# Performance work log

Measured on AMD Instinct MI355X. Metric: run time of the kernel, lower is better.

## Reference

```python
import jax, jax.numpy as jnp
import numpy as np

N_NODES = 100000
N_EDGES = 1600000
D = 64


def setup_inputs() -> dict:
    key = jax.random.key(0)
    ks = jax.random.split(key, 6)
    x = jax.random.normal(ks[0], (N_NODES, D), dtype=jnp.float32)
    edge_index = jax.random.randint(ks[1], (2, N_EDGES), 0, N_NODES, dtype=jnp.int64)
    W1 = jax.random.normal(ks[2], (D, D), dtype=jnp.float32) / np.sqrt(D)
    b1 = jax.random.normal(ks[3], (D,), dtype=jnp.float32) * 0.02
    W2 = jax.random.normal(ks[4], (D, D), dtype=jnp.float32) / np.sqrt(D)
    b2 = jax.random.normal(ks[5], (D,), dtype=jnp.float32) * 0.02
    return {"x": x, "edge_index": edge_index, "W1": W1, "b1": b1, "W2": W2, "b2": b2}


def _gcn_conv(x, W, b, src, dst, norm, n_nodes):
    # PyG GCNConv: h = X W; out_i = sum_{j->i} norm_ji * h_j; out += b
    h = x @ W                                   # [N, D]
    msgs = h[src] * norm[:, None]               # [E+N, D] gather
    out = jax.ops.segment_sum(msgs, dst, num_segments=n_nodes)  # scatter-add
    return out + b


def reference(x, edge_index, W1, b1, W2, b2):
    n = x.shape[0]
    # add self-loops (GCNConv default add_self_loops=True)
    loop = jnp.arange(n, dtype=edge_index.dtype)
    src = jnp.concatenate([edge_index[0], loop])
    dst = jnp.concatenate([edge_index[1], loop])
    # symmetric normalization D^{-1/2} (A+I) D^{-1/2}
    deg = jax.ops.segment_sum(jnp.ones_like(src, dtype=x.dtype), dst, num_segments=n)
    dinv = jax.lax.rsqrt(deg)                   # deg >= 1 due to self-loops
    norm = dinv[src] * dinv[dst]                # [E+N]
    h = _gcn_conv(x, W1, b1, src, dst, norm, n)
    h = jax.nn.relu(h)
    out = _gcn_conv(h, W2, b2, src, dst, norm, n)
    return out
```

## Files before the change

### kernel.cpp

```cpp
#include <hip/hip_runtime.h>

#define FDIM   64
#define BSHIFT 9
#define BNODES 512
#define BCAP   8960
#define EPB    4096
#define LPAD   72

typedef unsigned short bf16_t;
typedef __attribute__((ext_vector_type(8))) short bf16x8;
typedef __attribute__((ext_vector_type(4))) float f32x4;
typedef __attribute__((ext_vector_type(2))) float f32x2;

__device__ __forceinline__ unsigned f2bf(float f) {
    unsigned u = __float_as_uint(f);
    u += 0x7FFFu + ((u >> 16) & 1u);
    return u >> 16;
}
__device__ __forceinline__ float bflo(unsigned u) { return __uint_as_float(u << 16); }
__device__ __forceinline__ float bfhi(unsigned u) { return __uint_as_float(u & 0xFFFF0000u); }

__device__ __forceinline__ f32x2 bfpair(unsigned u) {
    f32x2 r;
    r.x = __uint_as_float(u << 16);
    r.y = __uint_as_float(u);
    return r;
}
__device__ __forceinline__ void addbf8p(f32x2* acc, uint4 v) {
    acc[0] += bfpair(v.x);
    acc[1] += bfpair(v.y);
    acc[2] += bfpair(v.z);
    acc[3] += bfpair(v.w);
}

__global__ void k_zero(int* __restrict__ g) { g[threadIdx.x] = 0; }

__global__ __launch_bounds__(256) void k_bucket(const int* __restrict__ src,
                                                const int* __restrict__ dst,
                                                int* __restrict__ gCursor,
                                                unsigned* __restrict__ pairs,
                                                int E, int N) {
    __shared__ int cnt4[4][256];
    __shared__ int cur4[4][256];
    const int t  = threadIdx.x;
    const int w  = t >> 6;
    const int e0 = blockIdx.x * EPB;
    int dcache[EPB / 256];
    #pragma unroll
    for (int i = 0; i < 4; ++i) cnt4[i][t] = 0;
    __syncthreads();

    #pragma unroll 4
    for (int i = 0; i < EPB / 256; ++i) {
        int e = e0 + i * 256 + t;
        int d = -1;
        if (e < E) {
            d = dst[e];
            d = min(max(d, 0), N - 1);
            atomicAdd(&cnt4[w][d >> BSHIFT], 1);
        }
        dcache[i] = d;
    }
    __syncthreads();
    {
        int c0 = cnt4[0][t], c1 = cnt4[1][t], c2 = cnt4[2][t], c3 = cnt4[3][t];
        int tot = c0 + c1 + c2 + c3;
        int b = 0;
        if (tot > 0) b = atomicAdd(&gCursor[t], tot);
        cur4[0][t] = b;
        cur4[1][t] = b + c0;
        cur4[2][t] = b + c0 + c1;
        cur4[3][t] = b + c0 + c1 + c2;
    }
    __syncthreads();
    #pragma unroll 4
    for (int i = 0; i < EPB / 256; ++i) {
        int d = dcache[i];
        if (d >= 0) {
            int e = e0 + i * 256 + t;
            int s = src[e];
            s = min(max(s, 0), N - 1);
            int bk = d >> BSHIFT;
            int slot = atomicAdd(&cur4[w][bk], 1);
            if (slot < BCAP)
                pairs[(size_t)bk * BCAP + slot] =
                    ((unsigned)(d & (BNODES - 1)) << 17) | (unsigned)s;
        }
    }
}

__global__ __launch_bounds__(1024) void k_sort(unsigned* __restrict__ pairs,
                                               const int* __restrict__ gCursor,
                                               float* __restrict__ dinv,
                                               int* __restrict__ beg,
                                               int* __restrict__ endp,
                                               int N) {
    __shared__ unsigned buf[BCAP];
    __shared__ int cnt4[4][BNODES];
    __shared__ int scn[BNODES];
    __shared__ int cur4[4][BNODES];
    const int b = blockIdx.x, t = threadIdx.x;
    const int grp = t >> 8;
    const int count = min(gCursor[b], BCAP);
    unsigned* p = pairs + (size_t)b * BCAP;

    ((int*)cnt4)[t] = 0;
    ((int*)cnt4)[t + 1024] = 0;
    __syncthreads();
    for (int i = t; i < count; i += 1024) {
        unsigned pk = p[i];
        buf[i] = pk;
        atomicAdd(&cnt4[grp][pk >> 17], 1);
    }
    __syncthreads();
    if (t < BNODES) scn[t] = cnt4[0][t] + cnt4[1][t] + cnt4[2][t] + cnt4[3][t];
    __syncthreads();
    for (int off = 1; off < BNODES; off <<= 1) {
        int v = 0;
        if (t < BNODES && t >= off) v = scn[t - off];
        __syncthreads();
        if (t < BNODES) scn[t] += v;
        __syncthreads();
    }
    if (t < BNODES) {
        int c0 = cnt4[0][t], c1 = cnt4[1][t], c2 = cnt4[2][t], c3 = cnt4[3][t];
        int tot = c0 + c1 + c2 + c3;
        int st  = scn[t] - tot;
        cur4[0][t] = st;
        cur4[1][t] = st + c0;
        cur4[2][t] = st + c0 + c1;
        cur4[3][t] = st + c0 + c1 + c2;
        int n = (b << BSHIFT) + t;
        if (n < N) {
            beg[n]  = b * BCAP + st;
            endp[n] = b * BCAP + st + tot;
            dinv[n] = rsqrtf((float)(tot + 1));
        }
    }
    __syncthreads();
    for (int i = t; i < count; i += 1024) {
        unsigned pk = buf[i];
        int pos = atomicAdd(&cur4[grp][pk >> 17], 1);
        p[pos] = pk & 0x1FFFFu;
    }
}

__device__ __forceinline__ void mfma_core(const bf16_t* Xs, const bf16_t* Wt,
                                          const float* __restrict__ dinv,
                                          bf16_t* __restrict__ Ob,
                                          int base, int N, int tid) {
    const int l  = tid & 63;
    const int w  = tid >> 6;
    const int lm = l & 15;
    const int lk = l >> 4;

    f32x4 acc[4];
    #pragma unroll
    for (int ct = 0; ct < 4; ++ct) acc[ct] = (f32x4){0.f, 0.f, 0.f, 0.f};

    #pragma unroll
    for (int kc = 0; kc < 2; ++kc) {
        bf16x8 a = *reinterpret_cast<const bf16x8*>(&Xs[(16 * w + lm) * LPAD + 32 * kc + 8 * lk]);
        #pragma unroll
        for (int ct = 0; ct < 4; ++ct) {
            bf16x8 b = *reinterpret_cast<const bf16x8*>(&Wt[(16 * ct + lm) * LPAD + 32 * kc + 8 * lk]);
            acc[ct] = __builtin_amdgcn_mfma_f32_16x16x32_bf16(a, b, acc[ct], 0, 0, 0);
        }
    }

    float dv[4];
    #pragma unroll
    for (int j = 0; j < 4; ++j) {
        int gr = base + 16 * w + 4 * lk + j;
        dv[j] = (gr < N) ? dinv[gr] : 0.f;
    }
    #pragma unroll
    for (int ct = 0; ct < 4; ++ct) {
        #pragma unroll
        for (int j = 0; j < 4; ++j) {
            int gr = base + 16 * w + 4 * lk + j;
            if (gr < N)
                Ob[(size_t)gr * FDIM + 16 * ct + lm] = (bf16_t)f2bf(acc[ct][j] * dv[j]);
        }
    }
}

__device__ __forceinline__ void stage_w_t(const float* __restrict__ W, bf16_t* Wt, int tid) {
    #pragma unroll
    for (int i = 0; i < 4; ++i) {
        int idx = tid + i * 256;
        int k  = idx >> 4;
        int c4 = (idx & 15) * 4;
        float4 v = reinterpret_cast<const float4*>(W)[idx];
        Wt[(c4 + 0) * LPAD + k] = (bf16_t)f2bf(v.x);
        Wt[(c4 + 1) * LPAD + k] = (bf16_t)f2bf(v.y);
        Wt[(c4 + 2) * LPAD + k] = (bf16_t)f2bf(v.z);
        Wt[(c4 + 3) * LPAD + k] = (bf16_t)f2bf(v.w);
    }
}

__global__ __launch_bounds__(256) void k_gemm_f32(const float* __restrict__ X,
                                                  const float* __restrict__ W,
                                                  const float* __restrict__ dinv,
                                                  bf16_t* __restrict__ Ob, int N) {
    __shared__ bf16_t Xs[64 * LPAD];
    __shared__ bf16_t Wt[64 * LPAD];
    const int tid  = threadIdx.x;
    const int base = blockIdx.x * 64;

    stage_w_t(W, Wt, tid);
    #pragma unroll
    for (int i = 0; i < 2; ++i) {
        int idx = tid + i * 256;
        int r = idx >> 3, c8 = (idx & 7) * 8;
        int gr = base + r;
        float4 v0 = make_float4(0.f, 0.f, 0.f, 0.f), v1 = v0;
        if (gr < N) {
            v0 = reinterpret_cast<const float4*>(X)[(size_t)gr * 16 + (idx & 7) * 2];
            v1 = reinterpret_cast<const float4*>(X)[(size_t)gr * 16 + (idx & 7) * 2 + 1];
        }
        uint4 o;
        o.x = f2bf(v0.x) | (f2bf(v0.y) << 16);
        o.y = f2bf(v0.z) | (f2bf(v0.w) << 16);
        o.z = f2bf(v1.x) | (f2bf(v1.y) << 16);
        o.w = f2bf(v1.z) | (f2bf(v1.w) << 16);
        *reinterpret_cast<uint4*>(&Xs[r * LPAD + c8]) = o;
    }
    __syncthreads();
    mfma_core(Xs, Wt, dinv, Ob, base, N, tid);
}

__global__ __launch_bounds__(256) void k_gemm_bf16(const bf16_t* __restrict__ Y,
                                                   const float* __restrict__ W,
                                                   const float* __restrict__ dinv,
                                                   bf16_t* __restrict__ Ob, int N) {
    __shared__ bf16_t Xs[64 * LPAD];
    __shared__ bf16_t Wt[64 * LPAD];
    const int tid  = threadIdx.x;
    const int base = blockIdx.x * 64;

    stage_w_t(W, Wt, tid);
    #pragma unroll
    for (int i = 0; i < 2; ++i) {
        int idx = tid + i * 256;
        int r = idx >> 3, c8 = (idx & 7) * 8;
        int gr = base + r;
        uint4 v = make_uint4(0u, 0u, 0u, 0u);
        if (gr < N) v = reinterpret_cast<const uint4*>(Y)[(size_t)gr * 8 + (idx & 7)];
        *reinterpret_cast<uint4*>(&Xs[r * LPAD + c8]) = v;
    }
    __syncthreads();
    mfma_core(Xs, Wt, dinv, Ob, base, N, tid);
}

__global__ __launch_bounds__(256) void k_agg(const bf16_t* __restrict__ Hs,
                                             const int* __restrict__ srcList,
                                             const int* __restrict__ beg,
                                             const int* __restrict__ endp,
                                             const float* __restrict__ dinv,
                                             const float* __restrict__ bias,
                                             float* __restrict__ Of,
                                             bf16_t* __restrict__ Ob,
                                             int N, int do_relu) {
    const int lane = threadIdx.x & 63;
    const int w    = threadIdx.x >> 6;
    const int g    = lane >> 3;
    const int c8   = lane & 7;
    const int nl   = g >> 1;
    const int par  = g & 1;
    const int node = (blockIdx.x * 4 + w) * 4 + nl;

    const uint4* Hv = reinterpret_cast<const uint4*>(Hs) + c8;

    int kb = 0, ke = 0;
    if (node < N) { kb = beg[node]; ke = endp[node]; }

    f32x2 acc[4];
    #pragma unroll
    for (int i = 0; i < 4; ++i) acc[i] = (f32x2){0.f, 0.f};

    int k = kb + par;
    for (; k + 6 < ke; k += 8) {
        int s0 = srcList[k],     s1 = srcList[k + 2];
        int s2 = srcList[k + 4], s3 = srcList[k + 6];
        uint4 h0 = Hv[(size_t)s0 * 8];
        uint4 h1 = Hv[(size_t)s1 * 8];
        uint4 h2 = Hv[(size_t)s2 * 8];
        uint4 h3 = Hv[(size_t)s3 * 8];
        addbf8p(acc, h0); addbf8p(acc, h1); addbf8p(acc, h2); addbf8p(acc, h3);
    }
    for (; k < ke; k += 2) {
        uint4 h0 = Hv[(size_t)srcList[k] * 8];
        addbf8p(acc, h0);
    }

    #pragma unroll
    for (int i = 0; i < 4; ++i) {
        acc[i].x += __shfl_xor(acc[i].x, 8, 64);
        acc[i].y += __shfl_xor(acc[i].y, 8, 64);
    }

    if (node >= N || par != 0) return;

    uint4 sv = Hv[(size_t)node * 8];
    acc[0].x += bflo(sv.x); acc[0].y += bfhi(sv.x);
    acc[1].x += bflo(sv.y); acc[1].y += bfhi(sv.y);
    acc[2].x += bflo(sv.z); acc[2].y += bfhi(sv.z);
    acc[3].x += bflo(sv.w); acc[3].y += bfhi(sv.w);

    const float di = dinv[node];
    const float4* bv = reinterpret_cast<const float4*>(bias);
    float4 b0 = bv[c8 * 2], b1 = bv[c8 * 2 + 1];
    float r[8];
    r[0] = fmaf(di, acc[0].x, b0.x); r[1] = fmaf(di, acc[0].y, b0.y);
    r[2] = fmaf(di, acc[1].x, b0.z); r[3] = fmaf(di, acc[1].y, b0.w);
    r[4] = fmaf(di, acc[2].x, b1.x); r[5] = fmaf(di, acc[2].y, b1.y);
    r[6] = fmaf(di, acc[3].x, b1.z); r[7] = fmaf(di, acc[3].y, b1.w);
    if (do_relu) {
        #pragma unroll
        for (int i = 0; i < 8; ++i) r[i] = fmaxf(r[i], 0.f);
    }
    if (Ob) {
        uint4 o;
        o.x = f2bf(r[0]) | (f2bf(r[1]) << 16);
        o.y = f2bf(r[2]) | (f2bf(r[3]) << 16);
        o.z = f2bf(r[4]) | (f2bf(r[5]) << 16);
        o.w = f2bf(r[6]) | (f2bf(r[7]) << 16);
        reinterpret_cast<uint4*>(Ob)[(size_t)node * 8 + c8] = o;
    } else {
        float4 o0 = make_float4(r[0], r[1], r[2], r[3]);
        float4 o1 = make_float4(r[4], r[5], r[6], r[7]);
        reinterpret_cast<float4*>(Of)[(size_t)node * 16 + c8 * 2]     = o0;
        reinterpret_cast<float4*>(Of)[(size_t)node * 16 + c8 * 2 + 1] = o1;
    }
}

extern "C" void kernel_launch(void* const* d_in, const int* in_sizes, int n_in,
                              void* d_out, int out_size, void* d_ws, size_t ws_size,
                              hipStream_t stream) {
    const float* x  = (const float*)d_in[0];
    const int*   ei = (const int*)  d_in[1];
    const float* W1 = (const float*)d_in[2];
    const float* b1 = (const float*)d_in[3];
    const float* W2 = (const float*)d_in[4];
    const float* b2 = (const float*)d_in[5];
    float* out = (float*)d_out;

    const int N = in_sizes[0] / FDIM;
    const int E = in_sizes[1] / 2;
    const int* src = ei;
    const int* dst = ei + E;

    const int nB = (N + BNODES - 1) >> BSHIFT;

    auto align1k = [](size_t v) { return (v + 1023) & ~(size_t)1023; };
    char* p = (char*)d_ws;
    int*      gCursor = (int*)p;        p += align1k(256 * 4);
    float*    dinv    = (float*)p;      p += align1k((size_t)N * 4);
    int*      beg     = (int*)p;        p += align1k((size_t)N * 4);
    int*      endp    = (int*)p;        p += align1k((size_t)N * 4);
    unsigned* pairs   = (unsigned*)p;   p += align1k((size_t)nB * BCAP * 4);
    bf16_t*   H       = (bf16_t*)p;     p += align1k((size_t)N * FDIM * 2);
    bf16_t*   Y       = (bf16_t*)p;

    k_zero<<<1, 256, 0, stream>>>(gCursor);
    k_bucket<<<(E + EPB - 1) / EPB, 256, 0, stream>>>(src, dst, gCursor, pairs, E, N);
    k_sort<<<nB, 1024, 0, stream>>>(pairs, gCursor, dinv, beg, endp, N);

    const int gemmBlocks = (N + 63) / 64;
    const int aggBlocks  = (N + 15) / 16;
    const int* srcList = (const int*)pairs;

    k_gemm_f32<<<gemmBlocks, 256, 0, stream>>>(x, W1, dinv, H, N);
    k_agg<<<aggBlocks, 256, 0, stream>>>(H, srcList, beg, endp, dinv, b1,
                                         nullptr, Y, N, 1);

    k_gemm_bf16<<<gemmBlocks, 256, 0, stream>>>(Y, W2, dinv, H, N);
    k_agg<<<aggBlocks, 256, 0, stream>>>(H, srcList, beg, endp, dinv, b2,
                                         out, nullptr, N, 0);
}
```

Baseline: 136.3 us.

## Assign one 8-lane group per node in aggregation and unroll gather by eight

```diff
diff --git a/kernel.cpp b/kernel.cpp
--- a/kernel.cpp
+++ b/kernel.cpp
@@ -266,9 +266,7 @@
     const int w    = threadIdx.x >> 6;
     const int g    = lane >> 3;
     const int c8   = lane & 7;
-    const int nl   = g >> 1;
-    const int par  = g & 1;
-    const int node = (blockIdx.x * 4 + w) * 4 + nl;
+    const int node = (blockIdx.x * 4 + w) * 8 + g;
 
     const uint4* Hv = reinterpret_cast<const uint4*>(Hs) + c8;
 
@@ -279,28 +277,39 @@
     #pragma unroll
     for (int i = 0; i < 4; ++i) acc[i] = (f32x2){0.f, 0.f};
 
-    int k = kb + par;
-    for (; k + 6 < ke; k += 8) {
-        int s0 = srcList[k],     s1 = srcList[k + 2];
-        int s2 = srcList[k + 4], s3 = srcList[k + 6];
+    int k = kb;
+    for (; k + 7 < ke; k += 8) {
+        int s0 = srcList[k],     s1 = srcList[k + 1];
+        int s2 = srcList[k + 2], s3 = srcList[k + 3];
+        int s4 = srcList[k + 4], s5 = srcList[k + 5];
+        int s6 = srcList[k + 6], s7 = srcList[k + 7];
+        uint4 h0 = Hv[(size_t)s0 * 8];
+        uint4 h1 = Hv[(size_t)s1 * 8];
+        uint4 h2 = Hv[(size_t)s2 * 8];
+        uint4 h3 = Hv[(size_t)s3 * 8];
+        uint4 h4 = Hv[(size_t)s4 * 8];
+        uint4 h5 = Hv[(size_t)s5 * 8];
+        uint4 h6 = Hv[(size_t)s6 * 8];
+        uint4 h7 = Hv[(size_t)s7 * 8];
+        addbf8p(acc, h0); addbf8p(acc, h1); addbf8p(acc, h2); addbf8p(acc, h3);
+        addbf8p(acc, h4); addbf8p(acc, h5); addbf8p(acc, h6); addbf8p(acc, h7);
+    }
+    if (k + 3 < ke) {
+        int s0 = srcList[k],     s1 = srcList[k + 1];
+        int s2 = srcList[k + 2], s3 = srcList[k + 3];
         uint4 h0 = Hv[(size_t)s0 * 8];
         uint4 h1 = Hv[(size_t)s1 * 8];
         uint4 h2 = Hv[(size_t)s2 * 8];
         uint4 h3 = Hv[(size_t)s3 * 8];
         addbf8p(acc, h0); addbf8p(acc, h1); addbf8p(acc, h2); addbf8p(acc, h3);
-    }
-    for (; k < ke; k += 2) {
+        k += 4;
+    }
+    for (; k < ke; ++k) {
         uint4 h0 = Hv[(size_t)srcList[k] * 8];
         addbf8p(acc, h0);
     }
 
-    #pragma unroll
-    for (int i = 0; i < 4; ++i) {
-        acc[i].x += __shfl_xor(acc[i].x, 8, 64);
-        acc[i].y += __shfl_xor(acc[i].y, 8, 64);
-    }
-
-    if (node >= N || par != 0) return;
+    if (node >= N) return;
 
     uint4 sv = Hv[(size_t)node * 8];
     acc[0].x += bflo(sv.x); acc[0].y += bfhi(sv.x);
@@ -368,7 +377,7 @@
     k_sort<<<nB, 1024, 0, stream>>>(pairs, gCursor, dinv, beg, endp, N);
 
     const int gemmBlocks = (N + 63) / 64;
-    const int aggBlocks  = (N + 15) / 16;
+    const int aggBlocks  = (N + 31) / 32;
     const int* srcList = (const int*)pairs;
 
     k_gemm_f32<<<gemmBlocks, 256, 0, stream>>>(x, W1, dinv, H, N);
```

Measured after the change: 137.0 us. No clear change (+0.6%).
